# Kernel tuning notes

Measured on AMD Instinct MI355X. Metric: run time of the kernel, lower is better.

The kernel has to match this reference:

```python
import jax, jax.numpy as jnp
import numpy as np

EPS_NORM = 1e-12   # F.normalize eps
EPS_SCALE = 1e-5   # activation scale clamp


def _weight_quant(w):
    # ternary (sign) quantization with mean-abs scale
    scale = jnp.mean(jnp.abs(w))
    u = jnp.sign(w - jnp.mean(w))
    return u, scale


def _activation_quant(x):
    # SimpleRMSNorm: l2-normalize over last dim, times dim**-0.5
    dim_scale = x.shape[-1] ** -0.5
    l2 = jnp.linalg.norm(x, axis=-1, keepdims=True)
    xn = x / jnp.maximum(l2, EPS_NORM) * dim_scale
    # per-token int8 scale
    scale = 127.0 / jnp.maximum(jnp.max(jnp.abs(xn), axis=-1, keepdims=True), EPS_SCALE)
    y = jnp.clip(jnp.round(xn * scale), -128.0, 127.0)
    return y, scale


def setup_inputs() -> dict:
    key = jax.random.key(0)
    kx, kw, kb = jax.random.split(key, 3)
    B, S, D, O = 4, 8192, 1024, 1024
    x = jax.random.normal(kx, (B, S, D), dtype=jnp.float32)
    w = jax.random.normal(kw, (O, D), dtype=jnp.float32)
    b = jax.random.normal(kb, (O,), dtype=jnp.float32)
    return {"x": x, "w": w, "b": b}


def reference(x, w, b):
    w_q, w_scale = _weight_quant(w)          # [O,D], scalar
    b_q, b_scale = _weight_quant(b)          # [O], scalar
    x_q, x_scale = _activation_quant(x)      # [B,S,D], [B,S,1]
    # mm + broadcast bias add, then dequant by product of all three scales
    y = jnp.einsum('bsd,od->bso', x_q, w_q) + b_q
    return y / (w_scale * x_scale * b_scale)
```

## Files before the change

kernel.cpp:

```cpp
#include <hip/hip_runtime.h>
#include <cstdint>
#include <cstddef>


typedef __attribute__((ext_vector_type(4))) int int4v;
typedef __attribute__((ext_vector_type(16))) int int16v;

static constexpr int DIM = 1024;
static constexpr int OUTF = 1024;
static constexpr int MROWS = 32768;
static constexpr float INV_WN = 1.0f / (1024.0f * 1024.0f);
static constexpr float INV_BN = 1.0f / 1024.0f;

#define OFF_XSCALE 1024
#define OFF_WQ 132096
#define OFF_XQ 1180672

__device__ inline float wave_sum(float v) {
#pragma unroll
  for (int off = 32; off; off >>= 1) v += __shfl_xor(v, off);
  return v;
}
__device__ inline float wave_max(float v) {
#pragma unroll
  for (int off = 32; off; off >>= 1) v = fmaxf(v, __shfl_xor(v, off));
  return v;
}

__global__ __launch_bounds__(256) void reduce_wb(const float* __restrict__ w,
                                                 const float* __restrict__ b,
                                                 float* __restrict__ red) {
  __shared__ float ss[4], sa[4];
  const int t = threadIdx.x;
  const int lane = t & 63, wv = t >> 6;
  float s = 0.0f, a = 0.0f;
  const float4* w4 = (const float4*)w;
  const int idx = blockIdx.x * 256 + t;
#pragma unroll
  for (int i = 0; i < 4; ++i) {
    float4 v = w4[idx + i * 65536];
    s += (v.x + v.y) + (v.z + v.w);
    a += (fabsf(v.x) + fabsf(v.y)) + (fabsf(v.z) + fabsf(v.w));
  }
  s = wave_sum(s);
  a = wave_sum(a);
  if (lane == 0) { ss[wv] = s; sa[wv] = a; }
  __syncthreads();
  if (t == 0) atomicAdd(&red[0], (ss[0] + ss[1]) + (ss[2] + ss[3]));
  if (t == 1) atomicAdd(&red[1], (sa[0] + sa[1]) + (sa[2] + sa[3]));
  if (blockIdx.x == 0) {
    __syncthreads();
    float4 v = ((const float4*)b)[t];
    float s2 = (v.x + v.y) + (v.z + v.w);
    float a2 = (fabsf(v.x) + fabsf(v.y)) + (fabsf(v.z) + fabsf(v.w));
    s2 = wave_sum(s2);
    a2 = wave_sum(a2);
    if (lane == 0) { ss[wv] = s2; sa[wv] = a2; }
    __syncthreads();
    if (t == 0) {
      red[2] = (ss[0] + ss[1]) + (ss[2] + ss[3]);
      red[3] = (sa[0] + sa[1]) + (sa[2] + sa[3]);
    }
  }
}

__global__ __launch_bounds__(256) void quant_w(const float* __restrict__ w,
                                               const float* __restrict__ red,
                                               signed char* __restrict__ wq) {
  const float wmean = red[0] * INV_WN;
  const int idx = blockIdx.x * 256 + threadIdx.x;
  float4 v = ((const float4*)w)[idx];
  int q0, q1, q2, q3;
  float d;
  d = v.x - wmean; q0 = d > 0.f ? 1 : (d < 0.f ? -1 : 0);
  d = v.y - wmean; q1 = d > 0.f ? 1 : (d < 0.f ? -1 : 0);
  d = v.z - wmean; q2 = d > 0.f ? 1 : (d < 0.f ? -1 : 0);
  d = v.w - wmean; q3 = d > 0.f ? 1 : (d < 0.f ? -1 : 0);
  const int pk = (q0 & 0xff) | ((q1 & 0xff) << 8) | ((q2 & 0xff) << 16) | ((q3 & 0xff) << 24);
  ((int*)wq)[idx] = pk;
}

__global__ __launch_bounds__(256) void quant_x(const float* __restrict__ x,
                                               signed char* __restrict__ xq,
                                               float* __restrict__ xscale) {
  const int wv = threadIdx.x >> 6;
  const int lane = threadIdx.x & 63;
  const int row = blockIdx.x * 4 + wv;
  const float4* xr = (const float4*)(x + (size_t)row * DIM);
  float4 v[4];
  float ss = 0.0f, ma = 0.0f;
#pragma unroll
  for (int it = 0; it < 4; ++it) {
    v[it] = xr[it * 64 + lane];
    ss += v[it].x * v[it].x + v[it].y * v[it].y + v[it].z * v[it].z + v[it].w * v[it].w;
    ma = fmaxf(ma, fmaxf(fmaxf(fabsf(v[it].x), fabsf(v[it].y)),
                         fmaxf(fabsf(v[it].z), fabsf(v[it].w))));
  }
  ss = wave_sum(ss);
  ma = wave_max(ma);

  const float l2 = sqrtf(ss);
  const float inv = 0.03125f / fmaxf(l2, 1e-12f);
  const float scale = 127.0f / fmaxf(ma * inv, 1e-5f);
  const float f = inv * scale;

  int* outp = (int*)(xq + (size_t)row * DIM);
#pragma unroll
  for (int it = 0; it < 4; ++it) {
    const int q0 = (int)fminf(fmaxf(rintf(v[it].x * f), -128.f), 127.f);
    const int q1 = (int)fminf(fmaxf(rintf(v[it].y * f), -128.f), 127.f);
    const int q2 = (int)fminf(fmaxf(rintf(v[it].z * f), -128.f), 127.f);
    const int q3 = (int)fminf(fmaxf(rintf(v[it].w * f), -128.f), 127.f);
    outp[it * 64 + lane] =
        (q0 & 0xff) | ((q1 & 0xff) << 8) | ((q2 & 0xff) << 16) | ((q3 & 0xff) << 24);
  }
  if (lane == 0) xscale[row] = scale;
}

__global__ __launch_bounds__(512, 2) void gemm_i8(
    const signed char* __restrict__ Aq,
    const signed char* __restrict__ Wq,
    const float* __restrict__ bias,
    const float* __restrict__ red,
    const float* __restrict__ xscale,
    float* __restrict__ out) {
  __shared__ signed char As[2][256 * 128];
  __shared__ signed char Bs[2][256 * 128];

  const int t = threadIdx.x;
  const int lane = t & 63;
  const int wv = t >> 6;
  const int l31 = lane & 31;
  const int hi = lane >> 5;
  const int wr = wv >> 2;
  const int wc = wv & 3;

  const int orig = blockIdx.x;
  const int swz = (orig & 7) * 64 + (orig >> 3);
  const int bn = swz & 3;
  const int bm = swz >> 2;

  const signed char* Ab = Aq + (size_t)bm * 256 * DIM;
  const signed char* Bb = Wq + (size_t)bn * 256 * DIM;

  const int ldsoff = lane * 16;
  const int row8 = lane >> 3;
  const int sw16 = (((lane & 7) ^ row8) << 4);

  int16v acc[4][2] = {};

#define STAGE(tt, dd)                                                            \
  do {                                                                           \
    const size_t koff_ = (size_t)(tt) * 128 + sw16;                              \
    _Pragma("unroll") for (int i_ = 0; i_ < 4; ++i_) {                           \
      const int blk_ = wv * 4 + i_;              \
      const size_t roff_ = (size_t)(blk_ * 8 + row8) * DIM + koff_;              \
      __builtin_amdgcn_global_load_lds(                                          \
          (const __attribute__((address_space(1))) void*)(Ab + roff_),           \
          (__attribute__((address_space(3))) void*)(&As[dd][blk_ * 1024 + ldsoff]), \
          16, 0, 0);                                                             \
      __builtin_amdgcn_global_load_lds(                                          \
          (const __attribute__((address_space(1))) void*)(Bb + roff_),           \
          (__attribute__((address_space(3))) void*)(&Bs[dd][blk_ * 1024 + ldsoff]), \
          16, 0, 0);                                                             \
    }                                                                            \
  } while (0)

#define COMPUTE(cc)                                                              \
  do {                                                                           \
    const int swr_ = (lane & 7) << 4;      \
    int4v bf[2][4];                                                              \
    _Pragma("unroll") for (int nf_ = 0; nf_ < 2; ++nf_) {                        \
      const int r_ = wc * 64 + nf_ * 32 + l31;                                   \
      _Pragma("unroll") for (int ks_ = 0; ks_ < 4; ++ks_)                        \
          bf[nf_][ks_] = *(const int4v*)&Bs[cc][r_ * 128 +                       \
                                                ((ks_ * 32 + hi * 16) ^ swr_)];  \
    }                                                                            \
    _Pragma("unroll") for (int mf_ = 0; mf_ < 4; ++mf_) {                        \
      int4v af[4];                                                               \
      const int r_ = wr * 128 + mf_ * 32 + l31;                                  \
      _Pragma("unroll") for (int ks_ = 0; ks_ < 4; ++ks_)                        \
          af[ks_] = *(const int4v*)&As[cc][r_ * 128 +                            \
                                           ((ks_ * 32 + hi * 16) ^ swr_)];       \
      __builtin_amdgcn_s_setprio(1);                                             \
      _Pragma("unroll") for (int nf_ = 0; nf_ < 2; ++nf_)                        \
          _Pragma("unroll") for (int ks_ = 0; ks_ < 4; ++ks_)                    \
              acc[mf_][nf_] = __builtin_amdgcn_mfma_i32_32x32x32_i8(             \
                  af[ks_], bf[nf_][ks_], acc[mf_][nf_], 0, 0, 0);                \
      __builtin_amdgcn_s_setprio(0);                                             \
    }                                                                            \
  } while (0)

  STAGE(0, 0);
#pragma unroll 1
  for (int tp = 0; tp < 4; ++tp) {
    STAGE(2 * tp + 1, 1);
    asm volatile("s_waitcnt vmcnt(8)" ::: "memory");
    asm volatile("s_barrier" ::: "memory");
    COMPUTE(0);
    asm volatile("s_barrier" ::: "memory");
    if (tp < 3) {
      STAGE(2 * tp + 2, 0);
      asm volatile("s_waitcnt vmcnt(8)" ::: "memory");
    } else {
      asm volatile("s_waitcnt vmcnt(0)" ::: "memory");
    }
    asm volatile("s_barrier" ::: "memory");
    COMPUTE(1);
    asm volatile("s_barrier" ::: "memory");
  }
#undef COMPUTE
#undef STAGE

  const float wscale = red[1] * INV_WN;
  const float bscale = red[3] * INV_BN;
  const float bmean = red[2] * INV_BN;
  const float wb = wscale * bscale;

  int bq[2];
#pragma unroll
  for (int nf = 0; nf < 2; ++nf) {
    const float bd = bias[bn * 256 + wc * 64 + nf * 32 + l31] - bmean;
    bq[nf] = bd > 0.f ? 1 : (bd < 0.f ? -1 : 0);
  }

#pragma unroll
  for (int mf = 0; mf < 4; ++mf) {
#pragma unroll
    for (int rq = 0; rq < 4; ++rq) {
      const int mg = bm * 256 + wr * 128 + mf * 32 + rq * 8 + hi * 4;
      const float4 xs = *(const float4*)&xscale[mg];
      float rec[4];
      rec[0] = 1.0f / (wb * xs.x);
      rec[1] = 1.0f / (wb * xs.y);
      rec[2] = 1.0f / (wb * xs.z);
      rec[3] = 1.0f / (wb * xs.w);
#pragma unroll
      for (int nf = 0; nf < 2; ++nf) {
        const int n = bn * 256 + wc * 64 + nf * 32 + l31;
#pragma unroll
        for (int rr = 0; rr < 4; ++rr) {
          const int reg = rq * 4 + rr;
          out[(size_t)(mg + rr) * OUTF + n] =
              (float)(acc[mf][nf][reg] + bq[nf]) * rec[rr];
        }
      }
    }
  }
}

extern "C" void kernel_launch(void* const* d_in, const int* in_sizes, int n_in,
                              void* d_out, int out_size, void* d_ws, size_t ws_size,
                              hipStream_t stream) {
  const float* x = (const float*)d_in[0];
  const float* w = (const float*)d_in[1];
  const float* b = (const float*)d_in[2];
  float* out = (float*)d_out;
  char* ws = (char*)d_ws;

  float* red = (float*)ws;
  float* xscale = (float*)(ws + OFF_XSCALE);
  signed char* wq = (signed char*)(ws + OFF_WQ);
  signed char* xq = (signed char*)(ws + OFF_XQ);

  hipMemsetAsync(red, 0, 4 * sizeof(float), stream);
  reduce_wb<<<256, 256, 0, stream>>>(w, b, red);
  quant_w<<<1024, 256, 0, stream>>>(w, red, wq);
  quant_x<<<MROWS / 4, 256, 0, stream>>>(x, xq, xscale);
  gemm_i8<<<dim3(512), 512, 0, stream>>>(xq, wq, b, red, xscale, out);
}
```

Measured before the change: 285.0 us.

## Replace atomic weight reduction with partials and restructure GEMM double-buffer pipeline

The weight sum and abs-sum now go to per-block partial arrays, which each quant_w block reduces itself, so the memset and float atomics are no longer needed. Block 0 writes the totals into red for the GEMM. Separately, the GEMM main loop is reordered: two stages are prefetched up front, each compute phase is followed by a full vmcnt(0) wait and barrier, and the next stage is then issued, which cuts barriers per iteration but changes how loads overlap with compute. The stricter vmcnt(0) waits may expose load latency, and the barrier placement before the overwriting STAGE needs to be correct.

```diff
diff --git a/kernel.cpp b/kernel.cpp
--- a/kernel.cpp
+++ b/kernel.cpp
@@ -15,6 +15,7 @@
 #define OFF_XSCALE 1024
 #define OFF_WQ 132096
 #define OFF_XQ 1180672
+#define OFF_PART 34735104
 
 __device__ inline float wave_sum(float v) {
 #pragma unroll
@@ -29,7 +30,8 @@
 
 __global__ __launch_bounds__(256) void reduce_wb(const float* __restrict__ w,
                                                  const float* __restrict__ b,
-                                                 float* __restrict__ red) {
+                                                 float* __restrict__ red,
+                                                 float* __restrict__ part) {
   __shared__ float ss[4], sa[4];
   const int t = threadIdx.x;
   const int lane = t & 63, wv = t >> 6;
@@ -46,8 +48,8 @@
   a = wave_sum(a);
   if (lane == 0) { ss[wv] = s; sa[wv] = a; }
   __syncthreads();
-  if (t == 0) atomicAdd(&red[0], (ss[0] + ss[1]) + (ss[2] + ss[3]));
-  if (t == 1) atomicAdd(&red[1], (sa[0] + sa[1]) + (sa[2] + sa[3]));
+  if (t == 0) part[blockIdx.x] = (ss[0] + ss[1]) + (ss[2] + ss[3]);
+  if (t == 1) part[256 + blockIdx.x] = (sa[0] + sa[1]) + (sa[2] + sa[3]);
   if (blockIdx.x == 0) {
     __syncthreads();
     float4 v = ((const float4*)b)[t];
@@ -65,10 +67,28 @@
 }
 
 __global__ __launch_bounds__(256) void quant_w(const float* __restrict__ w,
-                                               const float* __restrict__ red,
+                                               const float* __restrict__ part,
+                                               float* __restrict__ red,
                                                signed char* __restrict__ wq) {
-  const float wmean = red[0] * INV_WN;
-  const int idx = blockIdx.x * 256 + threadIdx.x;
+  __shared__ float smean;
+  const int t = threadIdx.x;
+  if (t < 64) {
+    float s = 0.0f;
+#pragma unroll
+    for (int i = 0; i < 4; ++i) s += part[t * 4 + i];
+    s = wave_sum(s);
+    if (t == 0) smean = s * INV_WN;
+    if (blockIdx.x == 0) {
+      float a = 0.0f;
+#pragma unroll
+      for (int i = 0; i < 4; ++i) a += part[256 + t * 4 + i];
+      a = wave_sum(a);
+      if (t == 0) { red[0] = s; red[1] = a; }
+    }
+  }
+  __syncthreads();
+  const float wmean = smean;
+  const int idx = blockIdx.x * 256 + t;
   float4 v = ((const float4*)w)[idx];
   int q0, q1, q2, q3;
   float d;
@@ -192,22 +212,21 @@
   } while (0)
 
   STAGE(0, 0);
+  STAGE(1, 1);
+  asm volatile("s_waitcnt vmcnt(8)" ::: "memory");
+  asm volatile("s_barrier" ::: "memory");
 #pragma unroll 1
   for (int tp = 0; tp < 4; ++tp) {
-    STAGE(2 * tp + 1, 1);
-    asm volatile("s_waitcnt vmcnt(8)" ::: "memory");
+    COMPUTE(0);
+    asm volatile("s_waitcnt vmcnt(0)" ::: "memory");
     asm volatile("s_barrier" ::: "memory");
-    COMPUTE(0);
-    asm volatile("s_barrier" ::: "memory");
+    if (tp < 3) STAGE(2 * tp + 2, 0);
+    COMPUTE(1);
     if (tp < 3) {
-      STAGE(2 * tp + 2, 0);
-      asm volatile("s_waitcnt vmcnt(8)" ::: "memory");
-    } else {
       asm volatile("s_waitcnt vmcnt(0)" ::: "memory");
-    }
-    asm volatile("s_barrier" ::: "memory");
-    COMPUTE(1);
-    asm volatile("s_barrier" ::: "memory");
+      asm volatile("s_barrier" ::: "memory");
+      STAGE(2 * tp + 3, 1);
+    }
   }
 #undef COMPUTE
 #undef STAGE
@@ -262,10 +281,10 @@
   float* xscale = (float*)(ws + OFF_XSCALE);
   signed char* wq = (signed char*)(ws + OFF_WQ);
   signed char* xq = (signed char*)(ws + OFF_XQ);
-
-  hipMemsetAsync(red, 0, 4 * sizeof(float), stream);
-  reduce_wb<<<256, 256, 0, stream>>>(w, b, red);
-  quant_w<<<1024, 256, 0, stream>>>(w, red, wq);
+  float* part = (float*)(ws + OFF_PART);
+
+  reduce_wb<<<256, 256, 0, stream>>>(w, b, red, part);
+  quant_w<<<1024, 256, 0, stream>>>(w, part, red, wq);
   quant_x<<<MROWS / 4, 256, 0, stream>>>(x, xq, xscale);
   gemm_i8<<<dim3(512), 512, 0, stream>>>(xq, wq, b, red, xscale, out);
 }
```

Result: faster. 274.7 us (-3.6%).
